# Optimization experiments

Hardware: AMD Instinct MI355X
Metric: run time of the kernel (lower is better)

Reference implementation:

```python
import jax, jax.numpy as jnp
import numpy as np

# DeformConv (RegSeg): offset conv + mask conv (sigmoid) + modulated deformable conv v2
STRIDE = 1
PAD = 1
DIL = 1
G = 1          # deformable_groups
KH, KW = 3, 3


def _conv(x, w, b):
    # standard NCHW conv, stride/pad/dilation of the module
    y = jax.lax.conv_general_dilated(
        x, w, window_strides=(STRIDE, STRIDE),
        padding=((PAD, PAD), (PAD, PAD)), rhs_dilation=(DIL, DIL),
        dimension_numbers=("NCHW", "OIHW", "NCHW"))
    return y + b[None, :, None, None]


def _deform_conv2d(x, offset, mask, w, b):
    # torchvision DeformConv2d (modulated, v2) semantics
    B, C, H, W = x.shape
    O = w.shape[0]
    K = KH * KW
    Ho = (H + 2 * PAD - DIL * (KH - 1) - 1) // STRIDE + 1
    Wo = (W + 2 * PAD - DIL * (KW - 1) - 1) // STRIDE + 1
    Cg = C // G

    # base sampling grid: p0 + p_k
    ky = jnp.repeat(jnp.arange(KH), KW) * DIL            # [K]
    kx = jnp.tile(jnp.arange(KW), KH) * DIL              # [K]
    oy = jnp.arange(Ho) * STRIDE - PAD                   # [Ho]
    ox = jnp.arange(Wo) * STRIDE - PAD                   # [Wo]
    base_y = (ky[:, None, None] + oy[None, :, None]).astype(x.dtype)  # [K,Ho,1]
    base_x = (kx[:, None, None] + ox[None, None, :]).astype(x.dtype)  # [K,1,Wo]

    off = offset.reshape(B, G, K, 2, Ho, Wo)             # channel layout: g, k, (dy,dx)
    py = base_y[None, None] + off[:, :, :, 0]            # [B,G,K,Ho,Wo]
    px = base_x[None, None] + off[:, :, :, 1]
    m = mask.reshape(B, G, K, Ho, Wo)

    imgf = x.reshape(B * G, Cg, H * W)
    y0 = jnp.floor(py).astype(jnp.int32)
    x0 = jnp.floor(px).astype(jnp.int32)
    ly = py - y0.astype(x.dtype)
    lx = px - x0.astype(x.dtype)

    def corner(iy, ix, wgt):
        # zero-padded bilinear corner: out-of-bounds corners contribute 0
        valid = (iy >= 0) & (iy < H) & (ix >= 0) & (ix < W)
        idx = (jnp.clip(iy, 0, H - 1) * W + jnp.clip(ix, 0, W - 1)).reshape(B * G, -1)
        g = jax.vmap(lambda im, ii: im[:, ii])(imgf, idx)            # [B*G,Cg,K*Ho*Wo]
        g = g.reshape(B, G, Cg, K, Ho, Wo)
        return g * (wgt * valid.astype(x.dtype))[:, :, None]          # [B,G,Cg,K,Ho,Wo]

    val = (corner(y0,     x0,     (1 - ly) * (1 - lx))
         + corner(y0,     x0 + 1, (1 - ly) * lx)
         + corner(y0 + 1, x0,     ly * (1 - lx))
         + corner(y0 + 1, x0 + 1, ly * lx))
    val = val * m[:, :, None]                                         # modulation

    wr = w.reshape(O, G, Cg, K)
    out = jnp.einsum("bgckpq,ogck->bopq", val, wr) + b[None, :, None, None]
    return out


def setup_inputs() -> dict:
    key = jax.random.key(0)
    ks = jax.random.split(key, 8)
    B, C, H, W, O = 4, 128, 96, 96, 128
    K = KH * KW
    fan = 1.0 / np.sqrt(C * K)
    return {
        "x":        jax.random.normal(ks[0], (B, C, H, W), jnp.float32),
        "x2":       jax.random.normal(ks[1], (B, C, H, W), jnp.float32),
        "offset_w": jax.random.normal(ks[2], (2 * G * K, C, KH, KW), jnp.float32) * 0.01,
        "offset_b": jax.random.normal(ks[3], (2 * G * K,), jnp.float32) * 0.01,
        "mask_w":   jax.random.normal(ks[4], (G * K, C, KH, KW), jnp.float32) * 0.05,
        "mask_b":   jnp.zeros((G * K,), jnp.float32),
        "deform_w": jax.random.normal(ks[5], (O, C, KH, KW), jnp.float32) * fan,
        "deform_b": jax.random.normal(ks[6], (O,), jnp.float32) * fan,
    }


def reference(x, x2, offset_w, offset_b, mask_w, mask_b, deform_w, deform_b):
    offset = _conv(x2, offset_w, offset_b)
    mask = jax.nn.sigmoid(_conv(x2, mask_w, mask_b))
    return _deform_conv2d(x, offset, mask, deform_w, deform_b)
```

## Files before the change

kernel.cpp:

```cpp
#include <hip/hip_runtime.h>

#define CIN   128
#define HH    96
#define WW    96
#define OUTC  128
#define HWSZ  9216
#define KK    9
#define KTOT  1152

typedef _Float16 f16x8 __attribute__((ext_vector_type(8)));
typedef _Float16 h2    __attribute__((ext_vector_type(2)));
typedef float    f32x4 __attribute__((ext_vector_type(4)));

__device__ __forceinline__ unsigned short f2h(float f) {
  _Float16 h = (_Float16)f;
  return __builtin_bit_cast(unsigned short, h);
}
__device__ __forceinline__ unsigned pack_h(float v0, float v1) {
  auto r = __builtin_amdgcn_cvt_pkrtz(v0, v1);
  return __builtin_bit_cast(unsigned, r);
}

#define WT2B_O 147456
#define BIAS_O 184320
#define XN_O   184384
#define X2N_O  (184384 + 4718592)

__global__ __launch_bounds__(256) void prep_all(
    const float* __restrict__ x, const float* __restrict__ x2,
    const float* __restrict__ offw, const float* __restrict__ maskw,
    const float* __restrict__ defw, const float* __restrict__ offb,
    const float* __restrict__ maskb, void* __restrict__ wsv) {
  int bid = blockIdx.x;
  int t = threadIdx.x;
  if (bid < 1152) {
    __shared__ unsigned short tile[64][136];
    int tsel = bid / 576;
    int rem = bid - tsel * 576;
    int b = rem / 144;
    int hw0 = (rem % 144) * 64;
    const float* src = tsel ? x2 : x;
    unsigned short* dst = (unsigned short*)wsv + (tsel ? X2N_O : XN_O);
    unsigned* tw = (unsigned*)&tile[0][0];
    int c2  = t & 15;
    int px4 = t >> 4;
#pragma unroll
    for (int pass = 0; pass < 4; ++pass) {
      int c = pass * 32 + c2 * 2;
      const float* r0 = src + ((size_t)(b * CIN + c)) * HWSZ + hw0 + px4 * 4;
      float4 f0 = *(const float4*)r0;
      float4 f1 = *(const float4*)(r0 + HWSZ);
      int wb = pass * 16 + c2;
      tw[(px4 * 4 + 0) * 68 + wb] = pack_h(f0.x, f1.x);
      tw[(px4 * 4 + 1) * 68 + wb] = pack_h(f0.y, f1.y);
      tw[(px4 * 4 + 2) * 68 + wb] = pack_h(f0.z, f1.z);
      tw[(px4 * 4 + 3) * 68 + wb] = pack_h(f0.w, f1.w);
    }
    __syncthreads();
    unsigned* drow = (unsigned*)(dst + ((size_t)(b * HWSZ + hw0)) * 128);
    int w4 = t & 15, pxr = t >> 4;
#pragma unroll
    for (int pass = 0; pass < 4; ++pass) {
      int px = pass * 16 + pxr;
      uint4 v = *(const uint4*)&tw[px * 68 + w4 * 4];
      *(uint4*)&drow[(size_t)px * 64 + w4 * 4] = v;
    }
    return;
  }
  unsigned short* wtb  = (unsigned short*)wsv;
  unsigned short* wt2b = wtb + WT2B_O;
  float* bias32 = (float*)(wtb + BIAS_O);
  int idx = (bid - 1152) * 256 + t;
  if (idx < OUTC * KTOT) {
    int o = idx / KTOT, r = idx - o * KTOT;
    int c = r / KK, tap = r - c * KK;
    wtb[o * KTOT + tap * 128 + c] = f2h(defw[idx]);
  } else if (idx < OUTC * KTOT + 32 * KTOT) {
    int j = idx - OUTC * KTOT;
    int oc = j / KTOT, r = j - oc * KTOT;
    int c = r / KK, tap = r - c * KK;
    float v = 0.f;
    if (oc < 18)      v = offw[j];
    else if (oc < 27) v = maskw[j - 18 * KTOT];
    wt2b[oc * KTOT + tap * 128 + c] = f2h(v);
  } else if (idx < OUTC * KTOT + 32 * KTOT + 32) {
    int j = idx - OUTC * KTOT - 32 * KTOT;
    float v = 0.f;
    if (j < 18) v = offb[j]; else if (j < 27) v = maskb[j - 18];
    bias32[j] = v;
  }
}

__global__ __launch_bounds__(256, 3) void fused(
    const float* __restrict__ defb, const void* __restrict__ wsv,
    float* __restrict__ out) {
  const unsigned short* wtb  = (const unsigned short*)wsv;
  const unsigned short* wt2b = wtb + WT2B_O;
  const float* bias32 = (const float*)(wtb + BIAS_O);
  const unsigned short* xn  = wtb + XN_O;
  const unsigned short* x2n = wtb + X2N_O;

  __shared__ unsigned bw[64 * 68];
  __shared__ unsigned short val[64][136];
  __shared__ unsigned sidxw[KK * 4 * 64];
  float* om = (float*)&val[0][0];

  int t = threadIdx.x;
  int w = t >> 6;
  int mw = w & 1, nw = w >> 1;
  int l15 = t & 15, quad = (t >> 4) & 3;
  int rb = blockIdx.x;
  int bid = (rb & 7) * 72 + (rb >> 3);
  int b = bid / 144;
  int pblk = (bid % 144) * 64;

  int phg[4], pwg[4];
#pragma unroll
  for (int G = 0; G < 4; ++G) {
    int p = pblk + w * 16 + G * 4 + quad;
    phg[G] = p / WW;
    pwg[G] = p - phg[G] * WW;
  }

  f32x4 oa0 = {0.f, 0.f, 0.f, 0.f};
  f32x4 oa1 = {0.f, 0.f, 0.f, 0.f};
  const unsigned short* x2nb = x2n + ((size_t)b * HWSZ) * 128;
  for (int tap = 0; tap < KK; ++tap) {
    int ky = tap / 3 - 1, kx = tap % 3 - 1;
    uint4 vG[4];
#pragma unroll
    for (int G = 0; G < 4; ++G) {
      int y = phg[G] + ky, xx = pwg[G] + kx;
      bool ok = ((unsigned)y < HH) && ((unsigned)xx < WW);
      int pos = ok ? (y * WW + xx) : 0;
      uint4 v = *(const uint4*)(x2nb + ((size_t)pos << 7) + l15 * 8);
      vG[G] = ok ? v : make_uint4(0u, 0u, 0u, 0u);
    }
#pragma unroll
    for (int j = 0; j < 2; ++j) {
      int cc = t + 256 * j;
      int row = cc >> 4, c16 = cc & 15;
      *(uint4*)&bw[row * 68 + c16 * 4] =
          *(const uint4*)(wt2b + (size_t)row * KTOT + tap * 128 + c16 * 8);
    }
#pragma unroll
    for (int G = 0; G < 4; ++G)
      *(uint4*)&val[w * 16 + G * 4 + quad][l15 * 8] = vG[G];
    __syncthreads();
#pragma unroll
    for (int ks = 0; ks < 4; ++ks) {
      f16x8 af = *(const f16x8*)&val[w * 16 + l15][ks * 32 + quad * 8];
      f16x8 b0 = *(const f16x8*)&bw[(size_t)l15 * 68 + ks * 16 + quad * 4];
      f16x8 b1 = *(const f16x8*)&bw[(size_t)(l15 + 16) * 68 + ks * 16 + quad * 4];
      oa0 = __builtin_amdgcn_mfma_f32_16x16x32_f16(af, b0, oa0, 0, 0, 0);
      oa1 = __builtin_amdgcn_mfma_f32_16x16x32_f16(af, b1, oa1, 0, 0, 0);
    }
    __syncthreads();
  }
#pragma unroll
  for (int nt = 0; nt < 2; ++nt) {
    f32x4 a = nt ? oa1 : oa0;
    int oc = nt * 16 + l15;
    float bia = bias32[oc];
#pragma unroll
    for (int r = 0; r < 4; ++r)
      om[oc * 68 + w * 16 + quad * 4 + r] = a[r] + bia;
  }
  __syncthreads();

  for (int e = t; e < KK * 64; e += 256) {
    int tap = e >> 6, pp = e & 63;
    int gp2 = pblk + pp;
    int h = gp2 / WW, ww_ = gp2 % WW;
    float dy = om[2 * tap * 68 + pp], dx = om[(2 * tap + 1) * 68 + pp];
    float mr = om[(18 + tap) * 68 + pp];
    float m = 1.f / (1.f + __expf(-mr));
    float py  = (float)(h + tap / 3 - 1) + dy;
    float pxx = (float)(ww_ + tap % 3 - 1) + dx;
    float y0f = floorf(py), x0f = floorf(pxx);
    int y0 = (int)y0f, x0 = (int)x0f;
    float ly = py - y0f, lx = pxx - x0f;
    int y1 = y0 + 1, x1 = x0 + 1;
    bool vy0 = (unsigned)y0 < HH, vy1 = (unsigned)y1 < HH;
    bool vx0 = (unsigned)x0 < WW, vx1 = (unsigned)x1 < WW;
    int cy0 = min(max(y0, 0), HH - 1), cy1 = min(max(y1, 0), HH - 1);
    int cx0 = min(max(x0, 0), WW - 1), cx1 = min(max(x1, 0), WW - 1);
    unsigned i00 = cy0 * WW + cx0, i01 = cy0 * WW + cx1;
    unsigned i10 = cy1 * WW + cx0, i11 = cy1 * WW + cx1;
    float w00 = (vy0 && vx0) ? m * (1.f - ly) * (1.f - lx) : 0.f;
    float w01 = (vy0 && vx1) ? m * (1.f - ly) * lx         : 0.f;
    float w10 = (vy1 && vx0) ? m * ly * (1.f - lx)         : 0.f;
    float w11 = (vy1 && vx1) ? m * ly * lx                 : 0.f;
    sidxw[(tap * 4 + 0) * 64 + pp] = i00 | ((unsigned)f2h(w00) << 16);
    sidxw[(tap * 4 + 1) * 64 + pp] = i01 | ((unsigned)f2h(w01) << 16);
    sidxw[(tap * 4 + 2) * 64 + pp] = i10 | ((unsigned)f2h(w10) << 16);
    sidxw[(tap * 4 + 3) * 64 + pp] = i11 | ((unsigned)f2h(w11) << 16);
  }
  __syncthreads();

  f32x4 acc[8];
#pragma unroll
  for (int nt = 0; nt < 8; ++nt) acc[nt] = (f32x4){0.f, 0.f, 0.f, 0.f};
  const unsigned short* xnb = xn + ((size_t)b * HWSZ) * 128;

  for (int tap = 0; tap < KK; ++tap) {
    unsigned sw[4][4];
#pragma unroll
    for (int cr = 0; cr < 4; ++cr)
#pragma unroll
      for (int G = 0; G < 4; ++G)
        sw[cr][G] = sidxw[(tap * 4 + cr) * 64 + w * 16 + G * 4 + quad];
    uint4 v[4][4];
#pragma unroll
    for (int G = 0; G < 4; ++G)
#pragma unroll
      for (int cr = 0; cr < 4; ++cr)
        v[cr][G] = *(const uint4*)(xnb + ((size_t)(sw[cr][G] & 0xffffu) << 7) + l15 * 8);
#pragma unroll
    for (int G = 0; G < 4; ++G) {
      h2 f[4];
#pragma unroll
      for (int j = 0; j < 4; ++j) f[j] = (h2){(_Float16)0.f, (_Float16)0.f};
#pragma unroll
      for (int cr = 0; cr < 4; ++cr) {
        _Float16 wh =
            __builtin_bit_cast(_Float16, (unsigned short)(sw[cr][G] >> 16));
        h2 wpk = {wh, wh};
        const h2* a = (const h2*)&v[cr][G];
#pragma unroll
        for (int j = 0; j < 4; ++j)
          f[j] += wpk * a[j];
      }
      *(uint4*)&val[w * 16 + G * 4 + quad][l15 * 8] =
          make_uint4(__builtin_bit_cast(unsigned, f[0]),
                     __builtin_bit_cast(unsigned, f[1]),
                     __builtin_bit_cast(unsigned, f[2]),
                     __builtin_bit_cast(unsigned, f[3]));
    }
#pragma unroll
    for (int j = 0; j < 4; ++j) {
      int cc = t + 256 * j;
      int row = cc >> 4, c16 = cc & 15;
      *(uint4*)&bw[row * 68 + c16 * 4] =
          *(const uint4*)(wtb + (size_t)row * KTOT + tap * 128 + c16 * 8);
    }
    __syncthreads();
    f16x8 af[2][4];
#pragma unroll
    for (int m = 0; m < 2; ++m)
#pragma unroll
      for (int ks = 0; ks < 4; ++ks)
        af[m][ks] =
            *(const f16x8*)&val[mw * 32 + m * 16 + l15][ks * 32 + quad * 8];
#pragma unroll
    for (int m = 0; m < 2; ++m)
#pragma unroll
      for (int ntl = 0; ntl < 2; ++ntl)
#pragma unroll
        for (int ks = 0; ks < 4; ++ks) {
          f16x8 bb = *(const f16x8*)&bw[(size_t)(nw * 32 + ntl * 16 + l15) * 68 +
                                        ks * 16 + quad * 4];
          acc[m * 2 + ntl] =
              __builtin_amdgcn_mfma_f32_16x16x32_f16(af[m][ks], bb,
                                                     acc[m * 2 + ntl], 0, 0, 0);
        }
    __syncthreads();
#pragma unroll
    for (int j = 0; j < 4; ++j) {
      int cc = t + 256 * j;
      int row = cc >> 4, c16 = cc & 15;
      *(uint4*)&bw[row * 68 + c16 * 4] =
          *(const uint4*)(wtb + (size_t)(64 + row) * KTOT + tap * 128 + c16 * 8);
    }
    __syncthreads();
#pragma unroll
    for (int m = 0; m < 2; ++m)
#pragma unroll
      for (int ntl = 0; ntl < 2; ++ntl)
#pragma unroll
        for (int ks = 0; ks < 4; ++ks) {
          f16x8 bb = *(const f16x8*)&bw[(size_t)(nw * 32 + ntl * 16 + l15) * 68 +
                                        ks * 16 + quad * 4];
          acc[4 + m * 2 + ntl] =
              __builtin_amdgcn_mfma_f32_16x16x32_f16(af[m][ks], bb,
                                                     acc[4 + m * 2 + ntl], 0, 0, 0);
        }
    __syncthreads();
  }

#pragma unroll
  for (int h = 0; h < 2; ++h)
#pragma unroll
    for (int m = 0; m < 2; ++m)
#pragma unroll
      for (int ntl = 0; ntl < 2; ++ntl) {
        int oc = h * 64 + nw * 32 + ntl * 16 + l15;
        f32x4 a = acc[h * 4 + m * 2 + ntl];
        float db = defb[oc];
        float4 vv = make_float4(a[0] + db, a[1] + db, a[2] + db, a[3] + db);
        *(float4*)&out[((size_t)b * OUTC + oc) * HWSZ + pblk + mw * 32 +
                       m * 16 + quad * 4] = vv;
      }
}

extern "C" void kernel_launch(void* const* d_in, const int* in_sizes, int n_in,
                              void* d_out, int out_size, void* d_ws, size_t ws_size,
                              hipStream_t stream) {
  const float* x     = (const float*)d_in[0];
  const float* x2    = (const float*)d_in[1];
  const float* offw  = (const float*)d_in[2];
  const float* offb  = (const float*)d_in[3];
  const float* maskw = (const float*)d_in[4];
  const float* maskb = (const float*)d_in[5];
  const float* defw  = (const float*)d_in[6];
  const float* defb  = (const float*)d_in[7];
  float* out = (float*)d_out;

  hipLaunchKernelGGL(prep_all, dim3(1873), dim3(256), 0, stream,
                     x, x2, offw, maskw, defw, offb, maskb, d_ws);
  hipLaunchKernelGGL(fused, dim3(576), dim3(256), 0, stream, defb, d_ws, out);
}
```

Before: 142.2 us.

## Double-buffer deform weights and prefetch next tap's gather during MFMA

Splits the weight staging buffer into two halves so the second output-channel half's weights load while the first half's MFMAs run. The next tap's bilinear gather loads are issued before the second half's MFMAs, hiding global latency behind compute. This also cuts the barriers per tap from four to two. In exchange it uses more LDS and registers, and launch bounds drop from 3 to 2 blocks per CU, which lowers occupancy.

```diff
diff --git a/kernel.cpp b/kernel.cpp
--- a/kernel.cpp
+++ b/kernel.cpp
@@ -91,7 +91,7 @@
   }
 }
 
-__global__ __launch_bounds__(256, 3) void fused(
+__global__ __launch_bounds__(256, 2) void fused(
     const float* __restrict__ defb, const void* __restrict__ wsv,
     float* __restrict__ out) {
   const unsigned short* wtb  = (const unsigned short*)wsv;
@@ -100,7 +100,8 @@
   const unsigned short* xn  = wtb + XN_O;
   const unsigned short* x2n = wtb + X2N_O;
 
-  __shared__ unsigned bw[64 * 68];
+  __shared__ unsigned bwA[64 * 68];
+  __shared__ unsigned bwB[64 * 68];
   __shared__ unsigned short val[64][136];
   __shared__ unsigned sidxw[KK * 4 * 64];
   float* om = (float*)&val[0][0];
@@ -140,7 +141,7 @@
     for (int j = 0; j < 2; ++j) {
       int cc = t + 256 * j;
       int row = cc >> 4, c16 = cc & 15;
-      *(uint4*)&bw[row * 68 + c16 * 4] =
+      *(uint4*)&bwA[row * 68 + c16 * 4] =
           *(const uint4*)(wt2b + (size_t)row * KTOT + tap * 128 + c16 * 8);
     }
 #pragma unroll
@@ -150,8 +151,8 @@
 #pragma unroll
     for (int ks = 0; ks < 4; ++ks) {
       f16x8 af = *(const f16x8*)&val[w * 16 + l15][ks * 32 + quad * 8];
-      f16x8 b0 = *(const f16x8*)&bw[(size_t)l15 * 68 + ks * 16 + quad * 4];
-      f16x8 b1 = *(const f16x8*)&bw[(size_t)(l15 + 16) * 68 + ks * 16 + quad * 4];
+      f16x8 b0 = *(const f16x8*)&bwA[(size_t)l15 * 68 + ks * 16 + quad * 4];
+      f16x8 b1 = *(const f16x8*)&bwA[(size_t)(l15 + 16) * 68 + ks * 16 + quad * 4];
       oa0 = __builtin_amdgcn_mfma_f32_16x16x32_f16(af, b0, oa0, 0, 0, 0);
       oa1 = __builtin_amdgcn_mfma_f32_16x16x32_f16(af, b1, oa1, 0, 0, 0);
     }
@@ -203,19 +204,19 @@
   for (int nt = 0; nt < 8; ++nt) acc[nt] = (f32x4){0.f, 0.f, 0.f, 0.f};
   const unsigned short* xnb = xn + ((size_t)b * HWSZ) * 128;
 
-  for (int tap = 0; tap < KK; ++tap) {
-    unsigned sw[4][4];
+  auto gatherT = [&](int tap, unsigned sw[4][4], uint4 v[4][4]) {
 #pragma unroll
     for (int cr = 0; cr < 4; ++cr)
 #pragma unroll
       for (int G = 0; G < 4; ++G)
         sw[cr][G] = sidxw[(tap * 4 + cr) * 64 + w * 16 + G * 4 + quad];
-    uint4 v[4][4];
 #pragma unroll
     for (int G = 0; G < 4; ++G)
 #pragma unroll
       for (int cr = 0; cr < 4; ++cr)
         v[cr][G] = *(const uint4*)(xnb + ((size_t)(sw[cr][G] & 0xffffu) << 7) + l15 * 8);
+  };
+  auto combineT = [&](unsigned sw[4][4], uint4 v[4][4]) {
 #pragma unroll
     for (int G = 0; G < 4; ++G) {
       h2 f[4];
@@ -237,14 +238,26 @@
                      __builtin_bit_cast(unsigned, f[2]),
                      __builtin_bit_cast(unsigned, f[3]));
     }
+  };
+  auto stageHalf = [&](unsigned* buf, int tap, int half) {
 #pragma unroll
     for (int j = 0; j < 4; ++j) {
       int cc = t + 256 * j;
       int row = cc >> 4, c16 = cc & 15;
-      *(uint4*)&bw[row * 68 + c16 * 4] =
-          *(const uint4*)(wtb + (size_t)row * KTOT + tap * 128 + c16 * 8);
-    }
-    __syncthreads();
+      *(uint4*)&buf[row * 68 + c16 * 4] =
+          *(const uint4*)(wtb + (size_t)(half * 64 + row) * KTOT + tap * 128 + c16 * 8);
+    }
+  };
+
+  {
+    unsigned sw[4][4]; uint4 v[4][4];
+    gatherT(0, sw, v);
+    combineT(sw, v);
+    stageHalf(bwA, 0, 0);
+  }
+  __syncthreads();
+
+  for (int tap = 0; tap < KK; ++tap) {
     f16x8 af[2][4];
 #pragma unroll
     for (int m = 0; m < 2; ++m)
@@ -252,40 +265,39 @@
       for (int ks = 0; ks < 4; ++ks)
         af[m][ks] =
             *(const f16x8*)&val[mw * 32 + m * 16 + l15][ks * 32 + quad * 8];
+    stageHalf(bwB, tap, 1);
 #pragma unroll
     for (int m = 0; m < 2; ++m)
 #pragma unroll
       for (int ntl = 0; ntl < 2; ++ntl)
 #pragma unroll
         for (int ks = 0; ks < 4; ++ks) {
-          f16x8 bb = *(const f16x8*)&bw[(size_t)(nw * 32 + ntl * 16 + l15) * 68 +
-                                        ks * 16 + quad * 4];
+          f16x8 bb = *(const f16x8*)&bwA[(size_t)(nw * 32 + ntl * 16 + l15) * 68 +
+                                         ks * 16 + quad * 4];
           acc[m * 2 + ntl] =
               __builtin_amdgcn_mfma_f32_16x16x32_f16(af[m][ks], bb,
                                                      acc[m * 2 + ntl], 0, 0, 0);
         }
     __syncthreads();
-#pragma unroll
-    for (int j = 0; j < 4; ++j) {
-      int cc = t + 256 * j;
-      int row = cc >> 4, c16 = cc & 15;
-      *(uint4*)&bw[row * 68 + c16 * 4] =
-          *(const uint4*)(wtb + (size_t)(64 + row) * KTOT + tap * 128 + c16 * 8);
-    }
-    __syncthreads();
+    unsigned sw[4][4]; uint4 v[4][4];
+    if (tap + 1 < KK) gatherT(tap + 1, sw, v);
 #pragma unroll
     for (int m = 0; m < 2; ++m)
 #pragma unroll
       for (int ntl = 0; ntl < 2; ++ntl)
 #pragma unroll
         for (int ks = 0; ks < 4; ++ks) {
-          f16x8 bb = *(const f16x8*)&bw[(size_t)(nw * 32 + ntl * 16 + l15) * 68 +
-                                        ks * 16 + quad * 4];
+          f16x8 bb = *(const f16x8*)&bwB[(size_t)(nw * 32 + ntl * 16 + l15) * 68 +
+                                         ks * 16 + quad * 4];
           acc[4 + m * 2 + ntl] =
               __builtin_amdgcn_mfma_f32_16x16x32_f16(af[m][ks], bb,
                                                      acc[4 + m * 2 + ntl], 0, 0, 0);
         }
-    __syncthreads();
+    if (tap + 1 < KK) {
+      combineT(sw, v);
+      stageHalf(bwA, tap + 1, 0);
+      __syncthreads();
+    }
   }
 
 #pragma unroll
```

After: 153.6 us. 8.0% more time.
